# Performance work log

Measured on AMD Instinct MI355X. Metric: run time of the kernel, lower is better.

## Reference

```python
import jax, jax.numpy as jnp
import numpy as np

DIM = 512
NUM_HEADS = 8
HEAD_DIM = DIM // NUM_HEADS
SCALE = HEAD_DIM ** -0.5


def _depthwise_s2(x, kernel):
    # DepthwiseConv2D(3, strides=2, padding='same') in NHWC; kernel [3,3,1,C]
    C = x.shape[-1]
    return jax.lax.conv_general_dilated(
        x, kernel, window_strides=(2, 2), padding='SAME',
        dimension_numbers=('NHWC', 'HWIO', 'NHWC'), feature_group_count=C)


def setup_inputs() -> dict:
    key = jax.random.key(0)
    ks = jax.random.split(key, 6)
    B, H, W = 2, 32, 32
    he = lambda k, shape, fan_in: jax.random.normal(k, shape, jnp.float32) * (2.0 / fan_in) ** 0.5
    return {
        'x': jax.random.normal(ks[0], (B, H, W, DIM), jnp.float32),
        'wq': he(ks[1], (DIM, DIM), DIM),
        'bq': jnp.zeros((DIM,), jnp.float32),
        'wkv': he(ks[2], (DIM, 2 * DIM), DIM),
        'bkv': jnp.zeros((2 * DIM,), jnp.float32),
        'dw_kernel': he(ks[3], (3, 3, 1, 2 * DIM), 9),
        'dw_bias': jnp.zeros((2 * DIM,), jnp.float32),
        'wo': he(ks[4], (DIM, DIM), DIM),
        'bo': jnp.zeros((DIM,), jnp.float32),
    }


def reference(x, wq, bq, wkv, bkv, dw_kernel, dw_bias, wo, bo):
    B, H, W, _ = x.shape
    q = x @ wq + bq                      # [B,H,W,DIM]
    kv = x @ wkv + bkv                   # [B,H,W,2*DIM]
    kv = _depthwise_s2(kv, dw_kernel) + dw_bias  # [B,H/2,W/2,2*DIM]
    kvh, kvw = kv.shape[1], kv.shape[2]
    k, v = jnp.split(kv, 2, axis=-1)     # each [B,kvh,kvw,DIM]
    L = H * W
    M = kvh * kvw * NUM_HEADS            # shared-KV length (channel fold)
    q = q.reshape(B, L, NUM_HEADS, HEAD_DIM)
    k = k.reshape(B, M, HEAD_DIM)        # single shared K head
    v = v.reshape(B, M, HEAD_DIM)        # single shared V head
    attn = jax.nn.softmax(jnp.einsum('blnd,bmd->bnlm', q, k) * SCALE, axis=-1)
    out = jnp.einsum('bnlm,bmd->blnd', attn, v).reshape(B, H, W, DIM)
    return out @ wo + bo
```

## Files before the change

### kernel.cpp

```cpp
#include <hip/hip_runtime.h>
#include <hip/hip_bf16.h>

#define DIMC   512
#define NHEADS 8
#define HD     64
#define Bb     2
#define Hh     32
#define Ww     32
#define Lq     1024
#define BHW    2048
#define KVH    16
#define KVW    16
#define Mkv    2048
#define SL2E   0.18033688011112042f
#define NC     4
#define NROWS  (Bb * NHEADS * Lq)

typedef short bf16x8_t __attribute__((ext_vector_type(8)));
typedef float f32x4_t  __attribute__((ext_vector_type(4)));

__device__ __forceinline__ short f2bf(float f) {
    __hip_bfloat16 h = __float2bfloat16(f);
    return *reinterpret_cast<short*>(&h);
}
__device__ __forceinline__ float bf2f(short s) {
    unsigned u = ((unsigned)(unsigned short)s) << 16;
    return *reinterpret_cast<float*>(&u);
}
__device__ __forceinline__ unsigned cvt_pk_bf16(float lo, float hi) {
    unsigned r;
    asm("v_cvt_pk_bf16_f32 %0, %1, %2" : "=v"(r) : "v"(lo), "v"(hi));
    return r;
}

#define QTILE 64
#define MTILE 64
#define ITERS (Mkv / NC / MTILE)

__global__ __launch_bounds__(256) void prep_k(
    const float* __restrict__ x, short* __restrict__ xb,
    const float* __restrict__ wq, const float* __restrict__ wkv,
    const float* __restrict__ wo, short* __restrict__ wqkvT,
    short* __restrict__ woT)
{
    const int z = blockIdx.z;
    if (z == 0) {
        const int i = (blockIdx.y * 32 + blockIdx.x) * 256 + threadIdx.x;
        const float4 f0 = reinterpret_cast<const float4*>(x)[i * 2 + 0];
        const float4 f1 = reinterpret_cast<const float4*>(x)[i * 2 + 1];
        bf16x8_t t;
        t[0]=f2bf(f0.x); t[1]=f2bf(f0.y); t[2]=f2bf(f0.z); t[3]=f2bf(f0.w);
        t[4]=f2bf(f1.x); t[5]=f2bf(f1.y); t[6]=f2bf(f1.z); t[7]=f2bf(f1.w);
        reinterpret_cast<bf16x8_t*>(xb)[i] = t;
        return;
    }
    const float* W; short* WT; int N, rbase;
    if (z == 1)      { W = wq;  WT = wqkvT; N = DIMC;     rbase = 0;   }
    else if (z == 2) { W = wkv; WT = wqkvT; N = 2 * DIMC; rbase = 512; }
    else             { W = wo;  WT = woT;   N = DIMC;     rbase = 0;   }
    const int n0 = blockIdx.x * 32, k0 = blockIdx.y * 32;
    if (n0 >= N) return;
    __shared__ float t[32][33];
    const int c = threadIdx.x & 31, r = threadIdx.x >> 5;
    #pragma unroll
    for (int i = 0; i < 4; ++i)
        t[r + 8 * i][c] = W[(size_t)(k0 + r + 8 * i) * N + n0 + c];
    __syncthreads();
    #pragma unroll
    for (int i = 0; i < 4; ++i)
        WT[(size_t)(rbase + n0 + r + 8 * i) * DIMC + k0 + c] = f2bf(t[c][r + 8 * i]);
}

__global__ __launch_bounds__(256) void gemm_qkv_k(
    const short* __restrict__ A, const short* __restrict__ WT,
    const float* __restrict__ bq, const float* __restrict__ bkv,
    short* __restrict__ qb, short* __restrict__ kvb)
{
    __shared__ __align__(16) char smem[32768];
    const int tid = threadIdx.x, w = tid >> 6, lane = tid & 63;
    const int lr = lane & 15, lg = lane >> 4;
    const int wm = w >> 1, wn = w & 1;
    const int m0 = blockIdx.y * 64;
    const int n0 = blockIdx.x * 64;

    const int sr = tid >> 2, sc = tid & 3;
    const short* Asrc = A  + (size_t)(m0 + sr) * DIMC + sc * 16;
    const short* Bsrc = WT + (size_t)(n0 + sr) * DIMC + sc * 16;
    bf16x8_t ar[2], br[2];
    auto load_stage = [&](int kc) {
        ar[0] = *reinterpret_cast<const bf16x8_t*>(Asrc + kc);
        ar[1] = *reinterpret_cast<const bf16x8_t*>(Asrc + kc + 8);
        br[0] = *reinterpret_cast<const bf16x8_t*>(Bsrc + kc);
        br[1] = *reinterpret_cast<const bf16x8_t*>(Bsrc + kc + 8);
    };
    const int rowb = sr * 128;
    const int swzw = (sr & 7) << 4;
    auto write_stage = [&](int bb) {
        char* S = smem + bb * 16384;
        *reinterpret_cast<bf16x8_t*>(S +        rowb + ((sc*32     ) ^ swzw)) = ar[0];
        *reinterpret_cast<bf16x8_t*>(S +        rowb + ((sc*32 + 16) ^ swzw)) = ar[1];
        *reinterpret_cast<bf16x8_t*>(S + 8192 + rowb + ((sc*32     ) ^ swzw)) = br[0];
        *reinterpret_cast<bf16x8_t*>(S + 8192 + rowb + ((sc*32 + 16) ^ swzw)) = br[1];
    };

    f32x4_t acc[2][2];
    #pragma unroll
    for (int i = 0; i < 2; ++i)
        #pragma unroll
        for (int j = 0; j < 2; ++j) acc[i][j] = f32x4_t{0.f,0.f,0.f,0.f};

    load_stage(0);
    write_stage(0);
    int cur = 0;

    for (int it = 0; it < 8; ++it) {
        __syncthreads();
        if (it < 7) load_stage((it + 1) * 64);

        char* S = smem + cur * 16384;
        bf16x8_t af[2][2], bf[2][2];
        #pragma unroll
        for (int s = 0; s < 2; ++s) {
            const int arow = wm * 32 + s * 16 + lr;
            const int brow = wn * 32 + s * 16 + lr;
            #pragma unroll
            for (int h = 0; h < 2; ++h) {
                af[s][h] = *reinterpret_cast<bf16x8_t*>(
                    S +        arow * 128 + ((h*64 + lg*16) ^ ((arow & 7) << 4)));
                bf[s][h] = *reinterpret_cast<bf16x8_t*>(
                    S + 8192 + brow * 128 + ((h*64 + lg*16) ^ ((brow & 7) << 4)));
            }
        }
        __builtin_amdgcn_s_setprio(1);
        #pragma unroll
        for (int ms = 0; ms < 2; ++ms)
            #pragma unroll
            for (int ns = 0; ns < 2; ++ns)
                #pragma unroll
                for (int h = 0; h < 2; ++h)
                    acc[ms][ns] = __builtin_amdgcn_mfma_f32_16x16x32_bf16(
                        af[ms][h], bf[ns][h], acc[ms][ns], 0, 0, 0);
        __builtin_amdgcn_s_setprio(0);

        if (it < 7) write_stage(cur ^ 1);
        cur ^= 1;
    }

    if (n0 < 512) {
        #pragma unroll
        for (int ns = 0; ns < 2; ++ns) {
            const int col = n0 + wn * 32 + ns * 16 + lr;
            const float bv = bq[col];
            #pragma unroll
            for (int ms = 0; ms < 2; ++ms) {
                const int row = m0 + wm * 32 + ms * 16 + lg * 4;
                #pragma unroll
                for (int j = 0; j < 4; ++j)
                    qb[(size_t)(row + j) * DIMC + col] = f2bf(acc[ms][ns][j] + bv);
            }
        }
    } else {
        #pragma unroll
        for (int ns = 0; ns < 2; ++ns) {
            const int col = n0 - 512 + wn * 32 + ns * 16 + lr;
            const float bv = bkv[col];
            #pragma unroll
            for (int ms = 0; ms < 2; ++ms) {
                const int row = m0 + wm * 32 + ms * 16 + lg * 4;
                #pragma unroll
                for (int j = 0; j < 4; ++j)
                    kvb[(size_t)(row + j) * 1024 + col] = f2bf(acc[ms][ns][j] + bv);
            }
        }
    }
}

__global__ __launch_bounds__(256) void dwconv_k(
    const short* __restrict__ kvb, const float* __restrict__ kern,
    const float* __restrict__ dbias, short* __restrict__ Kbf,
    short* __restrict__ Vt)
{
    const int idx = blockIdx.x * 256 + threadIdx.x;
    const int c0 = (idx & 127) * 8;
    const int ow = (idx >> 7) & 15;
    const int oh = (idx >> 11) & 15;
    const int b  = idx >> 15;

    float acc[8];
    {
        const float4 b0 = *reinterpret_cast<const float4*>(dbias + c0);
        const float4 b1 = *reinterpret_cast<const float4*>(dbias + c0 + 4);
        acc[0]=b0.x; acc[1]=b0.y; acc[2]=b0.z; acc[3]=b0.w;
        acc[4]=b1.x; acc[5]=b1.y; acc[6]=b1.z; acc[7]=b1.w;
    }
    #pragma unroll
    for (int kh = 0; kh < 3; ++kh) {
        const int ih = oh * 2 + kh;
        if (ih >= Hh) continue;
        #pragma unroll
        for (int kw = 0; kw < 3; ++kw) {
            const int iw = ow * 2 + kw;
            if (iw >= Ww) continue;
            const bf16x8_t v = *reinterpret_cast<const bf16x8_t*>(
                kvb + (((size_t)b * Hh + ih) * Ww + iw) * 1024 + c0);
            const float4 k0 = *reinterpret_cast<const float4*>(
                kern + (kh * 3 + kw) * 1024 + c0);
            const float4 k1 = *reinterpret_cast<const float4*>(
                kern + (kh * 3 + kw) * 1024 + c0 + 4);
            acc[0] += bf2f(v[0]) * k0.x; acc[1] += bf2f(v[1]) * k0.y;
            acc[2] += bf2f(v[2]) * k0.z; acc[3] += bf2f(v[3]) * k0.w;
            acc[4] += bf2f(v[4]) * k1.x; acc[5] += bf2f(v[5]) * k1.y;
            acc[6] += bf2f(v[6]) * k1.z; acc[7] += bf2f(v[7]) * k1.w;
        }
    }
    const int s = oh * KVW + ow;
    if (c0 < 512) {
        const int d = c0 & 63, ck = c0 >> 6;
        bf16x8_t r;
        #pragma unroll
        for (int j = 0; j < 8; ++j) r[j] = f2bf(acc[j]);
        *reinterpret_cast<bf16x8_t*>(
            Kbf + ((size_t)b * Mkv + s * 8 + ck) * HD + d) = r;
    } else {
        const int c2 = c0 - 512;
        const int d = c2 & 63, ck = c2 >> 6;
        const int m = s * 8 + ck;
        #pragma unroll
        for (int j = 0; j < 8; ++j)
            Vt[((size_t)b * HD + d + j) * Mkv + m] = f2bf(acc[j]);
    }
}

__global__ __launch_bounds__(256) void attn_mfma_k(
    const short* __restrict__ qb, const short* __restrict__ K,
    const short* __restrict__ Vt, short* __restrict__ po,
    float* __restrict__ pl)
{
    __shared__ __align__(16) char smem[40960];
    const int tid  = threadIdx.x;
    const int w    = tid >> 6;
    const int lane = tid & 63;
    char* Pl = smem + 32768 + w * 2048;
    const int bid = blockIdx.x;
    const int chunk = blockIdx.y;
    const int qt  = bid & 15;
    const int n   = (bid >> 4) & 7;
    const int b   = bid >> 7;
    const int q0  = qt * QTILE + w * 16;
    const int lr = lane & 15;
    const int lg = lane >> 4;

    bf16x8_t qf[2];
    {
        const short* qrow = qb + ((size_t)(b * Lq) + q0 + lr) * DIMC + n * HD + lg * 8;
        #pragma unroll
        for (int ks = 0; ks < 2; ++ks) {
            bf16x8_t t = *reinterpret_cast<const bf16x8_t*>(qrow + ks * 32);
            #pragma unroll
            for (int j = 0; j < 8; ++j) t[j] = f2bf(bf2f(t[j]) * SL2E);
            qf[ks] = t;
        }
    }

    f32x4_t o[4];
    #pragma unroll
    for (int dt = 0; dt < 4; ++dt) o[dt] = f32x4_t{0.f,0.f,0.f,0.f};
    float lacc[4] = {0.f,0.f,0.f,0.f};

    const short* Kb = K  + (size_t)b * Mkv * HD;
    const short* Vb = Vt + (size_t)b * HD * Mkv;
    const int mbase = chunk * (Mkv / NC);

    const int sr = tid >> 2;
    const int jc = tid & 3;
    bf16x8_t kreg[2], vreg[2];
    auto load_tile = [&](int mt) {
        #pragma unroll
        for (int i = 0; i < 2; ++i) {
            kreg[i] = *reinterpret_cast<const bf16x8_t*>(
                Kb + (size_t)(mt + sr) * HD + (jc + 4 * i) * 8);
            vreg[i] = *reinterpret_cast<const bf16x8_t*>(
                Vb + (size_t)sr * Mkv + mt + (jc + 4 * i) * 8);
        }
    };
    auto write_tile = [&](int bb) {
        char* Kl = smem + bb * 16384;
        char* Vl = smem + bb * 16384 + 8192;
        #pragma unroll
        for (int i = 0; i < 2; ++i) {
            const int off = sr * 128 + ((((jc + 4 * i) * 16)) ^ ((sr & 7) << 4));
            *reinterpret_cast<bf16x8_t*>(Kl + off) = kreg[i];
            *reinterpret_cast<bf16x8_t*>(Vl + off) = vreg[i];
        }
    };

    load_tile(mbase);
    write_tile(0);
    int cur = 0;

    const int pswz_r = ((lr & 7) << 4) ^ ((lr & 8) << 2);

    for (int it = 0; it < ITERS; ++it) {
        __syncthreads();
        if (it < ITERS - 1) load_tile(mbase + (it + 1) * MTILE);

        char* Kl = smem + cur * 16384;
        char* Vl = smem + cur * 16384 + 8192;

        bf16x8_t kf[4][2];
        #pragma unroll
        for (int nt = 0; nt < 4; ++nt) {
            const int ml = nt * 16 + lr;
            kf[nt][0] = *reinterpret_cast<bf16x8_t*>(
                Kl + ml * 128 + ((lg * 16)      ^ ((ml & 7) << 4)));
            kf[nt][1] = *reinterpret_cast<bf16x8_t*>(
                Kl + ml * 128 + ((64 + lg * 16) ^ ((ml & 7) << 4)));
        }
        f32x4_t s[4];
        #pragma unroll
        for (int nt = 0; nt < 4; ++nt) {
            f32x4_t acc = f32x4_t{0.f,0.f,0.f,0.f};
            acc = __builtin_amdgcn_mfma_f32_16x16x32_bf16(qf[0], kf[nt][0], acc, 0,0,0);
            acc = __builtin_amdgcn_mfma_f32_16x16x32_bf16(qf[1], kf[nt][1], acc, 0,0,0);
            s[nt] = acc;
        }
        #pragma unroll
        for (int nt = 0; nt < 4; ++nt)
            #pragma unroll
            for (int r = 0; r < 4; ++r) {
                float p = exp2f(s[nt][r]);
                s[nt][r] = p;
                lacc[r] += p;
            }

        #pragma unroll
        for (int r = 0; r < 4; ++r) {
            const unsigned pk01 = cvt_pk_bf16(s[0][r], s[1][r]);
            const unsigned pk23 = cvt_pk_bf16(s[2][r], s[3][r]);
            const int qL = lg * 4 + r;
            const int swzp = ((qL & 7) << 4) ^ ((qL & 8) << 2);
            char* prow = Pl + qL * 128;
            *reinterpret_cast<short*>(prow + ((lr * 2     ) ^ swzp)) = (short)pk01;
            *reinterpret_cast<short*>(prow + ((32 + lr * 2) ^ swzp)) = (short)(pk01 >> 16);
            *reinterpret_cast<short*>(prow + ((64 + lr * 2) ^ swzp)) = (short)pk23;
            *reinterpret_cast<short*>(prow + ((96 + lr * 2) ^ swzp)) = (short)(pk23 >> 16);
        }

        bf16x8_t vf[4][2], pf[2];
        #pragma unroll
        for (int dt = 0; dt < 4; ++dt) {
            const int dL = dt * 16 + lr;
            vf[dt][0] = *reinterpret_cast<bf16x8_t*>(
                Vl + dL * 128 + ((lg * 16)      ^ ((dL & 7) << 4)));
            vf[dt][1] = *reinterpret_cast<bf16x8_t*>(
                Vl + dL * 128 + ((64 + lg * 16) ^ ((dL & 7) << 4)));
        }
        #pragma unroll
        for (int ks2 = 0; ks2 < 2; ++ks2)
            pf[ks2] = *reinterpret_cast<bf16x8_t*>(
                Pl + lr * 128 + ((ks2 * 64 + lg * 16) ^ pswz_r));
        #pragma unroll
        for (int dt = 0; dt < 4; ++dt) {
            o[dt] = __builtin_amdgcn_mfma_f32_16x16x32_bf16(pf[0], vf[dt][0], o[dt], 0,0,0);
            o[dt] = __builtin_amdgcn_mfma_f32_16x16x32_bf16(pf[1], vf[dt][1], o[dt], 0,0,0);
        }

        if (it < ITERS - 1) write_tile(cur ^ 1);
        cur ^= 1;
    }

    #pragma unroll
    for (int r = 0; r < 4; ++r) {
        float l = lacc[r];
        l += __shfl_xor(l, 1);
        l += __shfl_xor(l, 2);
        l += __shfl_xor(l, 4);
        l += __shfl_xor(l, 8);
        const float inv = 1.0f / l;
        const int tok = (b << 10) + q0 + lg * 4 + r;
        const unsigned pk0 = cvt_pk_bf16(o[0][r] * inv, o[1][r] * inv);
        const unsigned pk1 = cvt_pk_bf16(o[2][r] * inv, o[3][r] * inv);
        short* pb = po + ((size_t)chunk * BHW + tok) * DIMC + (n << 6) + lr;
        pb[0]  = (short)pk0;  pb[16] = (short)(pk0 >> 16);
        pb[32] = (short)pk1;  pb[48] = (short)(pk1 >> 16);
        if (lr == 0)
            pl[chunk * NROWS + ((b * NHEADS + n) << 10) + q0 + lg * 4 + r] = l;
    }
}

__global__ __launch_bounds__(256) void gemm_out_k(
    const short* __restrict__ po, const float* __restrict__ pl,
    const short* __restrict__ WT, const float* __restrict__ bo,
    float* __restrict__ C)
{
    __shared__ __align__(16) char smem[24576];
    const int tid = threadIdx.x, w = tid >> 6, lane = tid & 63;
    const int lr = lane & 15, lg = lane >> 4;
    const int wm = w >> 1, wn = w & 1;
    const int m0 = blockIdx.y * 32;
    const int n0 = blockIdx.x * 64;

    const int sr = tid >> 3, scA = tid & 7;
    const int m  = m0 + sr;
    const int srB = tid >> 2, scB = tid & 3;
    const short* Bsrc = WT + (size_t)(n0 + srB) * DIMC + scB * 16;

    bf16x8_t pr[NC]; float lv[NC]; bf16x8_t br[2];
    auto load_stage = [&](int kc) {
        const int kg = kc + scA * 8;
        const int hn = kg >> 6;
        const int grow = ((m >> 10) * NHEADS + hn) * 1024 + (m & 1023);
        #pragma unroll
        for (int c = 0; c < NC; ++c) {
            pr[c] = *reinterpret_cast<const bf16x8_t*>(
                po + ((size_t)c * BHW + m) * DIMC + kg);
            lv[c] = pl[c * NROWS + grow];
        }
        br[0] = *reinterpret_cast<const bf16x8_t*>(Bsrc + kc);
        br[1] = *reinterpret_cast<const bf16x8_t*>(Bsrc + kc + 8);
    };
    auto write_stage = [&](int bb) {
        char* S = smem + bb * 12288;
        const float inv = 1.0f / (lv[0] + lv[1] + lv[2] + lv[3]);
        bf16x8_t av;
        #pragma unroll
        for (int j = 0; j < 8; ++j) {
            float s = lv[0]*bf2f(pr[0][j]) + lv[1]*bf2f(pr[1][j])
                    + lv[2]*bf2f(pr[2][j]) + lv[3]*bf2f(pr[3][j]);
            av[j] = f2bf(s * inv);
        }
        *reinterpret_cast<bf16x8_t*>(
            S + sr * 128 + ((scA * 16) ^ ((sr & 7) << 4))) = av;
        *reinterpret_cast<bf16x8_t*>(
            S + 4096 + srB * 128 + ((scB * 32)      ^ ((srB & 7) << 4))) = br[0];
        *reinterpret_cast<bf16x8_t*>(
            S + 4096 + srB * 128 + ((scB * 32 + 16) ^ ((srB & 7) << 4))) = br[1];
    };

    f32x4_t acc[2];
    acc[0] = f32x4_t{0.f,0.f,0.f,0.f};
    acc[1] = f32x4_t{0.f,0.f,0.f,0.f};

    load_stage(0);
    write_stage(0);
    int cur = 0;

    for (int it = 0; it < 8; ++it) {
        __syncthreads();
        if (it < 7) load_stage((it + 1) * 64);

        char* S = smem + cur * 12288;
        const int arow = wm * 16 + lr;
        bf16x8_t af[2], bfr[2][2];
        #pragma unroll
        for (int h = 0; h < 2; ++h) {
            af[h] = *reinterpret_cast<bf16x8_t*>(
                S + arow * 128 + ((h*64 + lg*16) ^ ((arow & 7) << 4)));
            #pragma unroll
            for (int ns = 0; ns < 2; ++ns) {
                const int brow = wn * 32 + ns * 16 + lr;
                bfr[ns][h] = *reinterpret_cast<bf16x8_t*>(
                    S + 4096 + brow * 128 + ((h*64 + lg*16) ^ ((brow & 7) << 4)));
            }
        }
        __builtin_amdgcn_s_setprio(1);
        #pragma unroll
        for (int ns = 0; ns < 2; ++ns)
            #pragma unroll
            for (int h = 0; h < 2; ++h)
                acc[ns] = __builtin_amdgcn_mfma_f32_16x16x32_bf16(
                    af[h], bfr[ns][h], acc[ns], 0, 0, 0);
        __builtin_amdgcn_s_setprio(0);

        if (it < 7) write_stage(cur ^ 1);
        cur ^= 1;
    }

    #pragma unroll
    for (int ns = 0; ns < 2; ++ns) {
        const int col = n0 + wn * 32 + ns * 16 + lr;
        const float bv = bo[col];
        const int row = m0 + wm * 16 + lg * 4;
        #pragma unroll
        for (int j = 0; j < 4; ++j)
            C[(size_t)(row + j) * DIMC + col] = acc[ns][j] + bv;
    }
}

extern "C" void kernel_launch(void* const* d_in, const int* in_sizes, int n_in,
                              void* d_out, int out_size, void* d_ws, size_t ws_size,
                              hipStream_t stream)
{
    const float* x    = (const float*)d_in[0];
    const float* wq   = (const float*)d_in[1];
    const float* bq   = (const float*)d_in[2];
    const float* wkv  = (const float*)d_in[3];
    const float* bkv  = (const float*)d_in[4];
    const float* dwk  = (const float*)d_in[5];
    const float* dwb  = (const float*)d_in[6];
    const float* wo   = (const float*)d_in[7];
    const float* bo   = (const float*)d_in[8];
    float* out = (float*)d_out;

    short* po    = (short*)d_ws;
    float* pl    = (float*)(po + (size_t)NC * BHW * DIMC);
    short* kvb   = (short*)d_ws;
    short* xb    = kvb + (size_t)BHW * 1024;
    short* wqkvT = (short*)(pl + (size_t)NC * NROWS);
    short* woT   = wqkvT + (size_t)3 * DIMC * DIMC;
    short* qb    = woT   + (size_t)DIMC * DIMC;
    short* Kbf   = qb    + (size_t)BHW * DIMC;
    short* Vt    = Kbf   + (size_t)Bb * Mkv * HD;

    prep_k<<<dim3(32, 16, 4), 256, 0, stream>>>(x, xb, wq, wkv, wo, wqkvT, woT);

    gemm_qkv_k<<<dim3(24, 32), 256, 0, stream>>>(xb, wqkvT, bq, bkv, qb, kvb);

    dwconv_k<<<256, 256, 0, stream>>>(kvb, dwk, dwb, Kbf, Vt);

    attn_mfma_k<<<dim3(Bb * NHEADS * (Lq / QTILE), NC), 256, 0, stream>>>(
        qb, Kbf, Vt, po, pl);

    gemm_out_k<<<dim3(8, 64), 256, 0, stream>>>(po, pl, woT, bo, out);
}
```

Baseline: 59.25 us.

## Load K/V fragments directly from global memory instead of LDS staging

The attention kernel stops staging K and V tiles through double-buffered shared memory with block-wide barriers. Each wave now loads its MFMA K and V fragments straight from global memory into registers, prefetching the next K tile while softmax runs. LDS shrinks to the per-wave P buffer, which may raise occupancy and removes the __syncthreads. The cost is that the four waves of a block each fetch the same K/V data redundantly, with less coalesced access, relying on L1/L2 hits.

```diff
diff --git a/kernel.cpp b/kernel.cpp
--- a/kernel.cpp
+++ b/kernel.cpp
@@ -236,11 +236,11 @@
     const short* __restrict__ Vt, short* __restrict__ po,
     float* __restrict__ pl)
 {
-    __shared__ __align__(16) char smem[40960];
+    __shared__ __align__(16) char smem[8192];
     const int tid  = threadIdx.x;
     const int w    = tid >> 6;
     const int lane = tid & 63;
-    char* Pl = smem + 32768 + w * 2048;
+    char* Pl = smem + w * 2048;
     const int bid = blockIdx.x;
     const int chunk = blockIdx.y;
     const int qt  = bid & 15;
@@ -271,51 +271,30 @@
     const short* Vb = Vt + (size_t)b * HD * Mkv;
     const int mbase = chunk * (Mkv / NC);
 
-    const int sr = tid >> 2;
-    const int jc = tid & 3;
-    bf16x8_t kreg[2], vreg[2];
-    auto load_tile = [&](int mt) {
-        #pragma unroll
-        for (int i = 0; i < 2; ++i) {
-            kreg[i] = *reinterpret_cast<const bf16x8_t*>(
-                Kb + (size_t)(mt + sr) * HD + (jc + 4 * i) * 8);
-            vreg[i] = *reinterpret_cast<const bf16x8_t*>(
-                Vb + (size_t)sr * Mkv + mt + (jc + 4 * i) * 8);
-        }
-    };
-    auto write_tile = [&](int bb) {
-        char* Kl = smem + bb * 16384;
-        char* Vl = smem + bb * 16384 + 8192;
-        #pragma unroll
-        for (int i = 0; i < 2; ++i) {
-            const int off = sr * 128 + ((((jc + 4 * i) * 16)) ^ ((sr & 7) << 4));
-            *reinterpret_cast<bf16x8_t*>(Kl + off) = kreg[i];
-            *reinterpret_cast<bf16x8_t*>(Vl + off) = vreg[i];
-        }
-    };
-
-    load_tile(mbase);
-    write_tile(0);
-    int cur = 0;
-
     const int pswz_r = ((lr & 7) << 4) ^ ((lr & 8) << 2);
 
+    const short* Krow = Kb + (size_t)lr * HD + lg * 8;
+    const short* Vrow = Vb + (size_t)(lr) * Mkv + lg * 8;
+
+    bf16x8_t kf[4][2];
+    #pragma unroll
+    for (int nt = 0; nt < 4; ++nt) {
+        const short* kp = Krow + (size_t)(mbase + nt * 16) * HD;
+        kf[nt][0] = *reinterpret_cast<const bf16x8_t*>(kp);
+        kf[nt][1] = *reinterpret_cast<const bf16x8_t*>(kp + 32);
+    }
+
     for (int it = 0; it < ITERS; ++it) {
-        __syncthreads();
-        if (it < ITERS - 1) load_tile(mbase + (it + 1) * MTILE);
-
-        char* Kl = smem + cur * 16384;
-        char* Vl = smem + cur * 16384 + 8192;
-
-        bf16x8_t kf[4][2];
-        #pragma unroll
-        for (int nt = 0; nt < 4; ++nt) {
-            const int ml = nt * 16 + lr;
-            kf[nt][0] = *reinterpret_cast<bf16x8_t*>(
-                Kl + ml * 128 + ((lg * 16)      ^ ((ml & 7) << 4)));
-            kf[nt][1] = *reinterpret_cast<bf16x8_t*>(
-                Kl + ml * 128 + ((64 + lg * 16) ^ ((ml & 7) << 4)));
-        }
+        const int mt = mbase + it * MTILE;
+
+        bf16x8_t vf[4][2];
+        #pragma unroll
+        for (int dt = 0; dt < 4; ++dt) {
+            const short* vp = Vrow + (size_t)(dt * 16) * Mkv + mt;
+            vf[dt][0] = *reinterpret_cast<const bf16x8_t*>(vp);
+            vf[dt][1] = *reinterpret_cast<const bf16x8_t*>(vp + 32);
+        }
+
         f32x4_t s[4];
         #pragma unroll
         for (int nt = 0; nt < 4; ++nt) {
@@ -324,6 +303,16 @@
             acc = __builtin_amdgcn_mfma_f32_16x16x32_bf16(qf[1], kf[nt][1], acc, 0,0,0);
             s[nt] = acc;
         }
+
+        if (it < ITERS - 1) {
+            #pragma unroll
+            for (int nt = 0; nt < 4; ++nt) {
+                const short* kp = Krow + (size_t)(mt + MTILE + nt * 16) * HD;
+                kf[nt][0] = *reinterpret_cast<const bf16x8_t*>(kp);
+                kf[nt][1] = *reinterpret_cast<const bf16x8_t*>(kp + 32);
+            }
+        }
+
         #pragma unroll
         for (int nt = 0; nt < 4; ++nt)
             #pragma unroll
@@ -345,28 +334,17 @@
             *reinterpret_cast<short*>(prow + ((64 + lr * 2) ^ swzp)) = (short)pk23;
             *reinterpret_cast<short*>(prow + ((96 + lr * 2) ^ swzp)) = (short)(pk23 >> 16);
         }
-
-        bf16x8_t vf[4][2], pf[2];
-        #pragma unroll
-        for (int dt = 0; dt < 4; ++dt) {
-            const int dL = dt * 16 + lr;
-            vf[dt][0] = *reinterpret_cast<bf16x8_t*>(
-                Vl + dL * 128 + ((lg * 16)      ^ ((dL & 7) << 4)));
-            vf[dt][1] = *reinterpret_cast<bf16x8_t*>(
-                Vl + dL * 128 + ((64 + lg * 16) ^ ((dL & 7) << 4)));
-        }
+        bf16x8_t pf[2];
         #pragma unroll
         for (int ks2 = 0; ks2 < 2; ++ks2)
             pf[ks2] = *reinterpret_cast<bf16x8_t*>(
                 Pl + lr * 128 + ((ks2 * 64 + lg * 16) ^ pswz_r));
+
         #pragma unroll
         for (int dt = 0; dt < 4; ++dt) {
             o[dt] = __builtin_amdgcn_mfma_f32_16x16x32_bf16(pf[0], vf[dt][0], o[dt], 0,0,0);
             o[dt] = __builtin_amdgcn_mfma_f32_16x16x32_bf16(pf[1], vf[dt][1], o[dt], 0,0,0);
         }
-
-        if (it < ITERS - 1) write_tile(cur ^ 1);
-        cur ^= 1;
     }
 
     #pragma unroll
```

Result: slower. 95.64 us (+61.4%).
